# Optimization experiments

Hardware: AMD Instinct MI355X
Metric: run time of the kernel (lower is better)

The kernel has to match this reference:

```python
import jax, jax.numpy as jnp
import numpy as np

BLOCK = 16           # NVFP4 block size along in_features
E2M1_MAX = 6.0       # max representable FP4 E2M1 magnitude
E4M3_MAX = 448.0     # max representable FP8 E4M3 magnitude
_TINY = 1e-30


def _quant_e2m1(x):
    """Round to nearest FP4 E2M1 value {0, +-0.5, 1, 1.5, 2, 3, 4, 6} (RNE)."""
    s = jnp.sign(x)
    ax = jnp.clip(jnp.abs(x), 0.0, E2M1_MAX)
    e = jnp.clip(jnp.floor(jnp.log2(jnp.maximum(ax, _TINY))), 0.0, 2.0)
    step = jnp.exp2(e)  # spacing within this binade is step/2 (1 mantissa bit)
    q = jnp.round(ax / step * 2.0) / 2.0 * step  # jnp.round = half-to-even
    return s * q


def _quant_e4m3(x):
    """Round to nearest FP8 E4M3 value (3 mantissa bits, subnormal min 2^-9)."""
    s = jnp.sign(x)
    ax = jnp.clip(jnp.abs(x), 0.0, E4M3_MAX)
    e = jnp.clip(jnp.floor(jnp.log2(jnp.maximum(ax, _TINY))), -6.0, 8.0)
    step = jnp.exp2(e)
    q = jnp.round(ax / step * 8.0) / 8.0 * step
    return s * q


def nvfp4_dequant_weight(weight, per_block_amax, global_amax):
    O, I = weight.shape
    nb = I // BLOCK
    # two-level scale: global fp32 scale + per-block E4M3 scale
    gscale = global_amax / (E2M1_MAX * E4M3_MAX)                 # scalar
    blk_scale_f = per_block_amax / E2M1_MAX                      # [O, nb]
    blk_scale = _quant_e4m3(blk_scale_f / gscale) * gscale       # [O, nb]
    wb = weight.reshape(O, nb, BLOCK)
    sb = blk_scale[:, :, None]
    wq = jnp.where(sb > 0, wb / jnp.maximum(sb, _TINY), 0.0)
    w_dq = _quant_e2m1(wq) * sb
    return w_dq.reshape(O, I)


def setup_inputs() -> dict:
    key = jax.random.key(0)
    kx, kw = jax.random.split(key)
    O, I, T = 4096, 4096, 8192
    x = jax.random.normal(kx, (T, I), dtype=jnp.float32)
    weight = jax.random.normal(kw, (O, I), dtype=jnp.float32)
    # amax values derived from the weight (static calibration)
    per_block_amax = jnp.max(jnp.abs(weight.reshape(O, I // BLOCK, BLOCK)), axis=-1)
    global_amax = jnp.max(jnp.abs(weight))
    return {"x": x, "weight": weight, "per_block_amax": per_block_amax,
            "global_amax": global_amax}


def reference(x, weight, per_block_amax, global_amax):
    w_dq = nvfp4_dequant_weight(weight, per_block_amax, global_amax)
    return jnp.matmul(x, w_dq.T)  # [T, O]
```

## Files before the change

kernel.cpp:

```cpp
#include <hip/hip_runtime.h>

typedef unsigned short u16;
typedef unsigned int u32;
typedef __attribute__((ext_vector_type(8))) __bf16 bf16x8;
typedef __attribute__((ext_vector_type(8))) unsigned short ushort8;
typedef __attribute__((ext_vector_type(4))) float f32x4;

__device__ __forceinline__ u16 f32_to_bf16(float f) {
  u32 u = __float_as_uint(f);
  u = (u + 0x7fffu + ((u >> 16) & 1u)) >> 16;
  return (u16)u;
}

__global__ void cvt_x_bf16(const float* __restrict__ x, u16* __restrict__ o, long n8) {
  long i = (long)blockIdx.x * blockDim.x + threadIdx.x;
  if (i >= n8) return;
  const float4* p = (const float4*)x + i * 2;
  float4 a = p[0], b = p[1];
  ushort8 v;
  v[0] = f32_to_bf16(a.x); v[1] = f32_to_bf16(a.y);
  v[2] = f32_to_bf16(a.z); v[3] = f32_to_bf16(a.w);
  v[4] = f32_to_bf16(b.x); v[5] = f32_to_bf16(b.y);
  v[6] = f32_to_bf16(b.z); v[7] = f32_to_bf16(b.w);
  *(ushort8*)(o + i * 8) = v;
}

__global__ void dequant_w(const float* __restrict__ w, const float* __restrict__ pba,
                          const float* __restrict__ gp, u16* __restrict__ wq, int nblk) {
  int i = blockIdx.x * blockDim.x + threadIdx.x;
  if (i >= nblk) return;
  float g = *gp;
  float gscale = g / 2688.0f;
  float ratio = (pba[i] / 6.0f) / gscale;
  ratio = fminf(fmaxf(ratio, 0.0f), 448.0f);
  int e = (int)((__float_as_uint(ratio) >> 23) & 0xffu) - 127;
  if (e < -6) e = -6;
  float stp = __uint_as_float((u32)(e - 3 + 127) << 23);
  float e4 = rintf(ratio / stp) * stp;
  float sb = e4 * gscale;
  float den = fmaxf(sb, 1e-30f);
  bool pos = sb > 0.0f;

  const float4* wp = (const float4*)(w + (size_t)i * 16);
  float vals[16];
#pragma unroll
  for (int t = 0; t < 4; ++t) {
    float4 v = wp[t];
    vals[4 * t + 0] = v.x; vals[4 * t + 1] = v.y;
    vals[4 * t + 2] = v.z; vals[4 * t + 3] = v.w;
  }
  ushort8 o0, o1;
#pragma unroll
  for (int k = 0; k < 16; ++k) {
    float wv = pos ? vals[k] / den : 0.0f;
    float s = (wv < 0.0f) ? -1.0f : 1.0f;
    float ax = fminf(fabsf(wv), 6.0f);
    float h = ax < 2.0f ? 0.5f : (ax < 4.0f ? 1.0f : 2.0f);
    float q = rintf(ax / h) * h;
    u16 r = f32_to_bf16(s * q * e4);
    if (k < 8) o0[k] = r; else o1[k - 8] = r;
  }
  ushort8* dst = (ushort8*)(wq + (size_t)i * 16);
  dst[0] = o0; dst[1] = o1;
}

#define GLL16(gp_, lp_)                                              \
  __builtin_amdgcn_global_load_lds(                                  \
      (__attribute__((address_space(1))) void*)(gp_),                \
      (__attribute__((address_space(3))) void*)(lp_), 16, 0, 0)

#define SBAR()                                   \
  do {                                           \
    __builtin_amdgcn_sched_barrier(0);           \
    __builtin_amdgcn_s_barrier();                \
    __builtin_amdgcn_sched_barrier(0);           \
  } while (0)

template <int VM, bool STG>
__device__ __forceinline__ void ktile(int t, u16 (&lds)[4][2][8192],
                                      const u16* gAs, const u16* gBs, size_t rh,
                                      int aro, int bro, int col8, int wave,
                                      f32x4 (&acc)[8][4]) {
  const u16* aL = &lds[t & 3][0][0];
  const u16* bL = &lds[t & 3][1][0];
  bf16x8 af[4], bv[4];
  if (STG) {
    u16* sd = &lds[(t + 3) & 3][0][wave * 512];
    const u16* g = gAs + (size_t)(t + 3) * 32;
    GLL16(g, sd);
    GLL16(g + rh, sd + 4096);
  }
#pragma unroll
  for (int m = 0; m < 4; ++m)
    af[m] = *(const bf16x8*)&aL[(aro + m * 16) * 32 + col8];
#pragma unroll
  for (int n = 0; n < 4; ++n)
    bv[n] = *(const bf16x8*)&bL[(bro + n * 16) * 32 + col8];
  SBAR();
  __builtin_amdgcn_s_setprio(1);
#pragma unroll
  for (int m = 0; m < 4; ++m)
#pragma unroll
    for (int n = 0; n < 4; ++n)
      acc[m][n] = __builtin_amdgcn_mfma_f32_16x16x32_bf16(af[m], bv[n], acc[m][n], 0, 0, 0);
  __builtin_amdgcn_s_setprio(0);
  SBAR();
  if (STG) {
    u16* sd = &lds[(t + 3) & 3][1][wave * 512];
    const u16* g = gBs + (size_t)(t + 3) * 32;
    GLL16(g, sd);
    GLL16(g + rh, sd + 4096);
  }
#pragma unroll
  for (int m = 0; m < 4; ++m)
    af[m] = *(const bf16x8*)&aL[(aro + 64 + m * 16) * 32 + col8];
  asm volatile("s_waitcnt vmcnt(%0)" ::"n"(VM) : "memory");
  SBAR();
  __builtin_amdgcn_s_setprio(1);
#pragma unroll
  for (int m = 0; m < 4; ++m)
#pragma unroll
    for (int n = 0; n < 4; ++n)
      acc[m + 4][n] =
          __builtin_amdgcn_mfma_f32_16x16x32_bf16(af[m], bv[n], acc[m + 4][n], 0, 0, 0);
  __builtin_amdgcn_s_setprio(0);
  SBAR();
}

__global__ __launch_bounds__(512, 2) void gemm_bt(
    const u16* __restrict__ A, const u16* __restrict__ B,
    float* __restrict__ C, const float* __restrict__ gp,
    int M, int N, int K) {
  __shared__ u16 lds[4][2][8192];
  const int tid = threadIdx.x;
  const int lane = tid & 63;
  const int wave = tid >> 6;

  const int bid = blockIdx.x;
  const int wg = (bid & 7) * 64 + (bid >> 3);
  const int bx = wg >> 5;
  const int by = wg & 31;
  const int m0 = by * 256;
  const int n0 = bx * 256;
  const int NK = K >> 5;

  f32x4 zero = {0.0f, 0.0f, 0.0f, 0.0f};
  f32x4 acc[8][4];
#pragma unroll
  for (int i = 0; i < 8; ++i)
#pragma unroll
    for (int j = 0; j < 4; ++j) acc[i][j] = zero;

  const int wrow = wave >> 2;
  const int wcol = wave & 3;

  const int srow = wave * 16 + (lane >> 2);
  const int scol = (((lane & 3) ^ ((lane >> 3) & 3)) << 3);
  const u16* gAs = A + (size_t)(m0 + srow) * K + scol;
  const u16* gBs = B + (size_t)(n0 + srow) * K + scol;
  const size_t rh = (size_t)128 * K;

  const int aro = wrow * 128 + (lane & 15);
  const int bro = wcol * 64 + (lane & 15);
  const int col8 = (((lane >> 4) ^ ((lane >> 1) & 3)) << 3);

#pragma unroll
  for (int t = 0; t < 3; ++t) {
    u16* dA = &lds[t][0][wave * 512];
    u16* dB = &lds[t][1][wave * 512];
    const u16* ga = gAs + (size_t)t * 32;
    const u16* gb = gBs + (size_t)t * 32;
    GLL16(ga, dA);
    GLL16(ga + rh, dA + 4096);
    GLL16(gb, dB);
    GLL16(gb + rh, dB + 4096);
  }
  asm volatile("s_waitcnt vmcnt(8)" ::: "memory");
  SBAR();

  int t = 0;
  for (; t < NK - 3; ++t)
    ktile<8, true>(t, lds, gAs, gBs, rh, aro, bro, col8, wave, acc);
  ktile<4, false>(t, lds, gAs, gBs, rh, aro, bro, col8, wave, acc); ++t;
  ktile<0, false>(t, lds, gAs, gBs, rh, aro, bro, col8, wave, acc); ++t;
  ktile<0, false>(t, lds, gAs, gBs, rh, aro, bro, col8, wave, acc);

  const float gs = (*gp) / 2688.0f;
  const int crow = m0 + wrow * 128 + ((lane >> 4) << 2);
  const int ccol = n0 + wcol * 64 + (lane & 15);
#pragma unroll
  for (int m = 0; m < 8; ++m)
#pragma unroll
    for (int r = 0; r < 4; ++r) {
      float* cp = C + (size_t)(crow + m * 16 + r) * N + ccol;
#pragma unroll
      for (int n = 0; n < 4; ++n) cp[n * 16] = acc[m][n][r] * gs;
    }
}

extern "C" void kernel_launch(void* const* d_in, const int* in_sizes, int n_in,
                              void* d_out, int out_size, void* d_ws, size_t ws_size,
                              hipStream_t stream) {
  const float* x   = (const float*)d_in[0];
  const float* w   = (const float*)d_in[1];
  const float* pba = (const float*)d_in[2];
  const float* gam = (const float*)d_in[3];
  float* out = (float*)d_out;

  const int T = 8192, I = 4096, O = 4096;
  u16* xb = (u16*)d_ws;
  u16* wb = xb + (size_t)T * I;

  long n8 = (long)T * I / 8;
  hipLaunchKernelGGL(cvt_x_bf16, dim3((unsigned)((n8 + 255) / 256)), dim3(256), 0, stream,
                     x, xb, n8);
  int nblk = O * (I / 16);
  hipLaunchKernelGGL(dequant_w, dim3(nblk / 256), dim3(256), 0, stream,
                     w, pba, gam, wb, nblk);
  hipLaunchKernelGGL(gemm_bt, dim3(O / 256 * (T / 256)), dim3(512), 0, stream,
                     xb, wb, out, gam, T, O, I);
}
```

Measured before the change: 538.6 us.

## Prefetch next k-tile LDS fragments into registers and narrow preprocessing threads

After: 503.6 us. -6.5%, faster.

```diff
diff --git a/kernel.cpp b/kernel.cpp
--- a/kernel.cpp
+++ b/kernel.cpp
@@ -3,7 +3,7 @@
 typedef unsigned short u16;
 typedef unsigned int u32;
 typedef __attribute__((ext_vector_type(8))) __bf16 bf16x8;
-typedef __attribute__((ext_vector_type(8))) unsigned short ushort8;
+typedef __attribute__((ext_vector_type(4))) unsigned short u16x4;
 typedef __attribute__((ext_vector_type(4))) float f32x4;
 
 __device__ __forceinline__ u16 f32_to_bf16(float f) {
@@ -12,23 +12,21 @@
   return (u16)u;
 }
 
-__global__ void cvt_x_bf16(const float* __restrict__ x, u16* __restrict__ o, long n8) {
+__global__ void cvt_x_bf16(const float* __restrict__ x, u16* __restrict__ o, long n4) {
   long i = (long)blockIdx.x * blockDim.x + threadIdx.x;
-  if (i >= n8) return;
-  const float4* p = (const float4*)x + i * 2;
-  float4 a = p[0], b = p[1];
-  ushort8 v;
+  if (i >= n4) return;
+  float4 a = ((const float4*)x)[i];
+  u16x4 v;
   v[0] = f32_to_bf16(a.x); v[1] = f32_to_bf16(a.y);
   v[2] = f32_to_bf16(a.z); v[3] = f32_to_bf16(a.w);
-  v[4] = f32_to_bf16(b.x); v[5] = f32_to_bf16(b.y);
-  v[6] = f32_to_bf16(b.z); v[7] = f32_to_bf16(b.w);
-  *(ushort8*)(o + i * 8) = v;
+  *(u16x4*)(o + i * 4) = v;
 }
 
 __global__ void dequant_w(const float* __restrict__ w, const float* __restrict__ pba,
-                          const float* __restrict__ gp, u16* __restrict__ wq, int nblk) {
-  int i = blockIdx.x * blockDim.x + threadIdx.x;
-  if (i >= nblk) return;
+                          const float* __restrict__ gp, u16* __restrict__ wq, int nth) {
+  int idx = blockIdx.x * blockDim.x + threadIdx.x;
+  if (idx >= nth) return;
+  int i = idx >> 2;
   float g = *gp;
   float gscale = g / 2688.0f;
   float ratio = (pba[i] / 6.0f) / gscale;
@@ -41,27 +39,19 @@
   float den = fmaxf(sb, 1e-30f);
   bool pos = sb > 0.0f;
 
-  const float4* wp = (const float4*)(w + (size_t)i * 16);
-  float vals[16];
-#pragma unroll
-  for (int t = 0; t < 4; ++t) {
-    float4 v = wp[t];
-    vals[4 * t + 0] = v.x; vals[4 * t + 1] = v.y;
-    vals[4 * t + 2] = v.z; vals[4 * t + 3] = v.w;
-  }
-  ushort8 o0, o1;
-#pragma unroll
-  for (int k = 0; k < 16; ++k) {
+  float4 v = ((const float4*)w)[idx];
+  float vals[4] = {v.x, v.y, v.z, v.w};
+  u16x4 o;
+#pragma unroll
+  for (int k = 0; k < 4; ++k) {
     float wv = pos ? vals[k] / den : 0.0f;
     float s = (wv < 0.0f) ? -1.0f : 1.0f;
     float ax = fminf(fabsf(wv), 6.0f);
     float h = ax < 2.0f ? 0.5f : (ax < 4.0f ? 1.0f : 2.0f);
     float q = rintf(ax / h) * h;
-    u16 r = f32_to_bf16(s * q * e4);
-    if (k < 8) o0[k] = r; else o1[k - 8] = r;
-  }
-  ushort8* dst = (ushort8*)(wq + (size_t)i * 16);
-  dst[0] = o0; dst[1] = o1;
+    o[k] = f32_to_bf16(s * q * e4);
+  }
+  *(u16x4*)(wq + (size_t)idx * 4) = o;
 }
 
 #define GLL16(gp_, lp_)                                              \
@@ -76,14 +66,16 @@
     __builtin_amdgcn_sched_barrier(0);           \
   } while (0)
 
-template <int VM, bool STG>
+template <int VM, bool STG, bool LAST>
 __device__ __forceinline__ void ktile(int t, u16 (&lds)[4][2][8192],
                                       const u16* gAs, const u16* gBs, size_t rh,
                                       int aro, int bro, int col8, int wave,
+                                      bf16x8 (&aC)[4], bf16x8 (&aN)[4],
+                                      bf16x8 (&bC)[4], bf16x8 (&bN)[4],
                                       f32x4 (&acc)[8][4]) {
   const u16* aL = &lds[t & 3][0][0];
-  const u16* bL = &lds[t & 3][1][0];
-  bf16x8 af[4], bv[4];
+  const u16* aL1 = &lds[(t + 1) & 3][0][0];
+  const u16* bL1 = &lds[(t + 1) & 3][1][0];
   if (STG) {
     u16* sd = &lds[(t + 3) & 3][0][wave * 512];
     const u16* g = gAs + (size_t)(t + 3) * 32;
@@ -92,17 +84,14 @@
   }
 #pragma unroll
   for (int m = 0; m < 4; ++m)
-    af[m] = *(const bf16x8*)&aL[(aro + m * 16) * 32 + col8];
-#pragma unroll
-  for (int n = 0; n < 4; ++n)
-    bv[n] = *(const bf16x8*)&bL[(bro + n * 16) * 32 + col8];
+    aN[m] = *(const bf16x8*)&aL[(aro + 64 + m * 16) * 32 + col8];
   SBAR();
   __builtin_amdgcn_s_setprio(1);
 #pragma unroll
   for (int m = 0; m < 4; ++m)
 #pragma unroll
     for (int n = 0; n < 4; ++n)
-      acc[m][n] = __builtin_amdgcn_mfma_f32_16x16x32_bf16(af[m], bv[n], acc[m][n], 0, 0, 0);
+      acc[m][n] = __builtin_amdgcn_mfma_f32_16x16x32_bf16(aC[m], bC[n], acc[m][n], 0, 0, 0);
   __builtin_amdgcn_s_setprio(0);
   SBAR();
   if (STG) {
@@ -111,18 +100,24 @@
     GLL16(g, sd);
     GLL16(g + rh, sd + 4096);
   }
-#pragma unroll
-  for (int m = 0; m < 4; ++m)
-    af[m] = *(const bf16x8*)&aL[(aro + 64 + m * 16) * 32 + col8];
-  asm volatile("s_waitcnt vmcnt(%0)" ::"n"(VM) : "memory");
-  SBAR();
+  if (!LAST) asm volatile("s_waitcnt vmcnt(%0)" ::"n"(VM) : "memory");
+  SBAR();
+  if (!LAST) {
+#pragma unroll
+    for (int m = 0; m < 4; ++m)
+      aC[m] = *(const bf16x8*)&aL1[(aro + m * 16) * 32 + col8];
+#pragma unroll
+    for (int n = 0; n < 4; ++n)
+      bN[n] = *(const bf16x8*)&bL1[(bro + n * 16) * 32 + col8];
+    __builtin_amdgcn_sched_barrier(0);
+  }
   __builtin_amdgcn_s_setprio(1);
 #pragma unroll
   for (int m = 0; m < 4; ++m)
 #pragma unroll
     for (int n = 0; n < 4; ++n)
       acc[m + 4][n] =
-          __builtin_amdgcn_mfma_f32_16x16x32_bf16(af[m], bv[n], acc[m + 4][n], 0, 0, 0);
+          __builtin_amdgcn_mfma_f32_16x16x32_bf16(aN[m], bC[n], acc[m + 4][n], 0, 0, 0);
   __builtin_amdgcn_s_setprio(0);
   SBAR();
 }
@@ -178,12 +173,23 @@
   asm volatile("s_waitcnt vmcnt(8)" ::: "memory");
   SBAR();
 
+  bf16x8 aC[4], aN[4], bC[4], bN[4];
+#pragma unroll
+  for (int m = 0; m < 4; ++m)
+    aC[m] = *(const bf16x8*)&lds[0][0][(aro + m * 16) * 32 + col8];
+#pragma unroll
+  for (int n = 0; n < 4; ++n)
+    bC[n] = *(const bf16x8*)&lds[0][1][(bro + n * 16) * 32 + col8];
+
   int t = 0;
-  for (; t < NK - 3; ++t)
-    ktile<8, true>(t, lds, gAs, gBs, rh, aro, bro, col8, wave, acc);
-  ktile<4, false>(t, lds, gAs, gBs, rh, aro, bro, col8, wave, acc); ++t;
-  ktile<0, false>(t, lds, gAs, gBs, rh, aro, bro, col8, wave, acc); ++t;
-  ktile<0, false>(t, lds, gAs, gBs, rh, aro, bro, col8, wave, acc);
+  for (; t < NK - 4; t += 2) {
+    ktile<8, true, false>(t, lds, gAs, gBs, rh, aro, bro, col8, wave, aC, aN, bC, bN, acc);
+    ktile<8, true, false>(t + 1, lds, gAs, gBs, rh, aro, bro, col8, wave, aC, aN, bN, bC, acc);
+  }
+  ktile<8, true,  false>(t,     lds, gAs, gBs, rh, aro, bro, col8, wave, aC, aN, bC, bN, acc);
+  ktile<4, false, false>(t + 1, lds, gAs, gBs, rh, aro, bro, col8, wave, aC, aN, bN, bC, acc);
+  ktile<0, false, false>(t + 2, lds, gAs, gBs, rh, aro, bro, col8, wave, aC, aN, bC, bN, acc);
+  ktile<0, false, true >(t + 3, lds, gAs, gBs, rh, aro, bro, col8, wave, aC, aN, bN, bC, acc);
 
   const float gs = (*gp) / 2688.0f;
   const int crow = m0 + wrow * 128 + ((lane >> 4) << 2);
@@ -211,12 +217,12 @@
   u16* xb = (u16*)d_ws;
   u16* wb = xb + (size_t)T * I;
 
-  long n8 = (long)T * I / 8;
-  hipLaunchKernelGGL(cvt_x_bf16, dim3((unsigned)((n8 + 255) / 256)), dim3(256), 0, stream,
-                     x, xb, n8);
-  int nblk = O * (I / 16);
-  hipLaunchKernelGGL(dequant_w, dim3(nblk / 256), dim3(256), 0, stream,
-                     w, pba, gam, wb, nblk);
+  long n4 = (long)T * I / 4;
+  hipLaunchKernelGGL(cvt_x_bf16, dim3((unsigned)((n4 + 255) / 256)), dim3(256), 0, stream,
+                     x, xb, n4);
+  int nth = O * (I / 16) * 4;
+  hipLaunchKernelGGL(dequant_w, dim3(nth / 256), dim3(256), 0, stream,
+                     w, pba, gam, wb, nth);
   hipLaunchKernelGGL(gemm_bt, dim3(O / 256 * (T / 256)), dim3(512), 0, stream,
                      xb, wb, out, gam, T, O, I);
 }
```
